# Kernel optimization log

Hardware: AMD Instinct MI355X
Metric: run time of the kernel (lower is better)

The kernel has to match this reference:

```python
import jax, jax.numpy as jnp
import numpy as np

SIGMA = 1.0  # init kwarg: Gaussian kernel width

B, P, F = 8192, 8192, 256


def setup_inputs() -> dict:
    key = jax.random.key(0)
    kx, kp = jax.random.split(key)
    x = jax.random.normal(kx, (B, F), dtype=jnp.float32)
    prototypes = jax.random.normal(kp, (P, F), dtype=jnp.float32)
    return {"x": x, "prototypes": prototypes}


def reference(x, prototypes):
    x_sq = jnp.sum(x * x, axis=-1, keepdims=True)            # [B,1]
    p_sq = jnp.sum(prototypes * prototypes, axis=-1)          # [P]
    cross = jnp.einsum('bf,pf->bp', x, prototypes)            # [B,P]
    d2 = jnp.maximum(x_sq + p_sq[None, :] - 2.0 * cross, 0.0)
    # NOTE: original takes .pow(0.5) -> euclidean NORM (despite variable name)
    dist = jnp.sqrt(d2)                                       # [B,P]
    denom = jnp.float32(2.0 * SIGMA ** 2)
    return jnp.exp(-dist / denom)
```

## Files before the change

### kernel.cpp

```cpp
#include <hip/hip_runtime.h>
#include <cstdint>
#include <cstddef>

#define B_ROWS 8192
#define P_ROWS 8192
#define FDIM   256

#define BM 128
#define BN 128
#define BK 64
#define NSTEP (FDIM / BK)

typedef __bf16  bf16x8  __attribute__((ext_vector_type(8)));
typedef float   floatx4 __attribute__((ext_vector_type(4)));

__device__ __forceinline__ unsigned short f2bf(float f) {
  unsigned int u = __float_as_uint(f);
  u += 0x7fffu + ((u >> 16) & 1u);
  return (unsigned short)(u >> 16);
}

__device__ __forceinline__ void async16(const void* g, void* l) {
  __builtin_amdgcn_global_load_lds(
      (const __attribute__((address_space(1))) void*)g,
      (__attribute__((address_space(3))) void*)l,
      16, 0, 0);
}

__global__ void __launch_bounds__(64) prep_kernel(
    const float* __restrict__ x, const float* __restrict__ p,
    unsigned short* __restrict__ xbf, unsigned short* __restrict__ pbf,
    float* __restrict__ x2, float* __restrict__ p2) {
  const int row  = blockIdx.x;
  const int lane = threadIdx.x;

  const float* src;
  unsigned short* dst;
  float* nrm;
  int r;
  if (row < B_ROWS) { src = x; dst = xbf; nrm = x2; r = row; }
  else              { src = p; dst = pbf; nrm = p2; r = row - B_ROWS; }

  const float4 v = *reinterpret_cast<const float4*>(src + (size_t)r * FDIM + lane * 4);
  float s = v.x * v.x + v.y * v.y + v.z * v.z + v.w * v.w;
  #pragma unroll
  for (int o = 32; o > 0; o >>= 1) s += __shfl_down(s, o);
  if (lane == 0) nrm[r] = s;

  ushort4 pk;
  pk.x = f2bf(v.x); pk.y = f2bf(v.y); pk.z = f2bf(v.z); pk.w = f2bf(v.w);
  *reinterpret_cast<ushort4*>(dst + (size_t)r * FDIM + lane * 4) = pk;
}

__global__ void __launch_bounds__(256) gauss_kernel(
    const unsigned short* __restrict__ xbf, const unsigned short* __restrict__ pbf,
    const float* __restrict__ x2, const float* __restrict__ p2,
    float* __restrict__ out) {
  __shared__ __align__(16) unsigned short lds_a[BM * BK];
  __shared__ __align__(16) unsigned short lds_b[BN * BK];

  const int t    = threadIdx.x;
  const int lane = t & 63;
  const int w    = t >> 6;
  const int wr   = w >> 1;
  const int wc   = w & 1;
  const int lm   = lane & 15;
  const int q    = lane >> 4;
  const int sx   = lane & 7;

  const int M0 = blockIdx.y * BM;
  const int N0 = blockIdx.x * BN;

  const unsigned short* aSrc[4];
  const unsigned short* bSrc[4];
  int ldsOff[4];
  #pragma unroll
  for (int I = 0; I < 4; ++I) {
    const int L = I * 256 + w * 64 + lane;
    const int r = L >> 3;
    const int c = L & 7;
    const int g = c ^ (r & 7);
    aSrc[I] = xbf + (size_t)(M0 + r) * FDIM + g * 8;
    bSrc[I] = pbf + (size_t)(N0 + r) * FDIM + g * 8;
    ldsOff[I] = (I * 256 + w * 64) * 8;
  }

  floatx4 acc[4][4] = {};

  for (int s = 0; s < NSTEP; ++s) {
    __syncthreads();
    #pragma unroll
    for (int I = 0; I < 4; ++I) async16(aSrc[I] + s * BK, &lds_a[ldsOff[I]]);
    #pragma unroll
    for (int I = 0; I < 4; ++I) async16(bSrc[I] + s * BK, &lds_b[ldsOff[I]]);
    __syncthreads();

    #pragma unroll
    for (int kk = 0; kk < 2; ++kk) {
      const int slot = ((kk * 4 + q) ^ sx) * 8;
      const int aoff = (wr * 64 + lm) * BK + slot;
      const int boff = (wc * 64 + lm) * BK + slot;
      bf16x8 af[4], bfr[4];
      #pragma unroll
      for (int i = 0; i < 4; ++i) af[i]  = *(const bf16x8*)&lds_a[aoff + i * 16 * BK];
      #pragma unroll
      for (int j = 0; j < 4; ++j) bfr[j] = *(const bf16x8*)&lds_b[boff + j * 16 * BK];
      #pragma unroll
      for (int i = 0; i < 4; ++i)
        #pragma unroll
        for (int j = 0; j < 4; ++j)
          acc[i][j] = __builtin_amdgcn_mfma_f32_16x16x32_bf16(af[i], bfr[j], acc[i][j], 0, 0, 0);
    }
  }

  float p2r[4];
  #pragma unroll
  for (int j = 0; j < 4; ++j) p2r[j] = p2[N0 + wc * 64 + j * 16 + lm];
  float x2r[16];
  #pragma unroll
  for (int i = 0; i < 4; ++i)
    #pragma unroll
    for (int v = 0; v < 4; ++v)
      x2r[i * 4 + v] = x2[M0 + wr * 64 + i * 16 + q * 4 + v];

  #pragma unroll
  for (int i = 0; i < 4; ++i) {
    const int mbase = M0 + wr * 64 + i * 16 + q * 4;
    #pragma unroll
    for (int v = 0; v < 4; ++v) {
      float* orow = out + (size_t)(mbase + v) * P_ROWS + N0 + wc * 64 + lm;
      #pragma unroll
      for (int j = 0; j < 4; ++j) {
        float d2 = x2r[i * 4 + v] + p2r[j] - 2.0f * acc[i][j][v];
        d2 = fmaxf(d2, 0.0f);
        const float dist = sqrtf(d2);
        orow[j * 16] = __expf(-0.5f * dist);
      }
    }
  }
}

extern "C" void kernel_launch(void* const* d_in, const int* in_sizes, int n_in,
                              void* d_out, int out_size, void* d_ws, size_t ws_size,
                              hipStream_t stream) {
  const float* x = (const float*)d_in[0];
  const float* p = (const float*)d_in[1];
  float* out = (float*)d_out;

  char* ws = (char*)d_ws;
  unsigned short* xbf = (unsigned short*)ws;
  unsigned short* pbf = (unsigned short*)(ws + (size_t)B_ROWS * FDIM * 2);
  float* x2 = (float*)(ws + (size_t)(B_ROWS + P_ROWS) * FDIM * 2);
  float* p2 = x2 + B_ROWS;

  prep_kernel<<<dim3(B_ROWS + P_ROWS), dim3(64), 0, stream>>>(x, p, xbf, pbf, x2, p2);

  dim3 grid(P_ROWS / BN, B_ROWS / BM);
  gauss_kernel<<<grid, dim3(256), 0, stream>>>(xbf, pbf, x2, p2, out);
}
```

Baseline: 302.2 us.

## Permute prototype rows for vectorized nontemporal stores and XCD-aware block swizzle

Loads B-tile rows in a permuted order so that each lane's MFMA output columns are contiguous, which lets the epilogue write float4 values with nontemporal stores instead of scalar strided stores. The x2/p2 norm loads become vector loads as well. Block indices are remapped so that blocks landing on the same XCD share M tiles for better L2 reuse. The launch bounds ask for 4 blocks per SIMD-occupancy target, which may constrain registers.

Result: no change. 300.7 us (-0.5%).

```diff
diff --git a/kernel.cpp b/kernel.cpp
--- a/kernel.cpp
+++ b/kernel.cpp
@@ -52,7 +52,7 @@
   *reinterpret_cast<ushort4*>(dst + (size_t)r * FDIM + lane * 4) = pk;
 }
 
-__global__ void __launch_bounds__(256) gauss_kernel(
+__global__ void __launch_bounds__(256, 4) gauss_kernel(
     const unsigned short* __restrict__ xbf, const unsigned short* __restrict__ pbf,
     const float* __restrict__ x2, const float* __restrict__ p2,
     float* __restrict__ out) {
@@ -68,11 +68,13 @@
   const int q    = lane >> 4;
   const int sx   = lane & 7;
 
-  const int M0 = blockIdx.y * BM;
-  const int N0 = blockIdx.x * BN;
+  const int f   = blockIdx.y * 64 + blockIdx.x;
+  const int xcd = f & 7;
+  const int i2  = f >> 3;
+  const int M0  = (xcd * 8 + (i2 & 7)) * BM;
+  const int N0  = (i2 >> 3) * BN;
 
-  const unsigned short* aSrc[4];
-  const unsigned short* bSrc[4];
+  unsigned int aOff[4], bOff[4];
   int ldsOff[4];
   #pragma unroll
   for (int I = 0; I < 4; ++I) {
@@ -80,8 +82,9 @@
     const int r = L >> 3;
     const int c = L & 7;
     const int g = c ^ (r & 7);
-    aSrc[I] = xbf + (size_t)(M0 + r) * FDIM + g * 8;
-    bSrc[I] = pbf + (size_t)(N0 + r) * FDIM + g * 8;
+    aOff[I] = (unsigned int)((M0 + r) * FDIM + g * 8);
+    const int pr = (r & 64) + 4 * (r & 15) + ((r >> 4) & 3);
+    bOff[I] = (unsigned int)((N0 + pr) * FDIM + g * 8);
     ldsOff[I] = (I * 256 + w * 64) * 8;
   }
 
@@ -90,9 +93,9 @@
   for (int s = 0; s < NSTEP; ++s) {
     __syncthreads();
     #pragma unroll
-    for (int I = 0; I < 4; ++I) async16(aSrc[I] + s * BK, &lds_a[ldsOff[I]]);
+    for (int I = 0; I < 4; ++I) async16(xbf + aOff[I] + s * BK, &lds_a[ldsOff[I]]);
     #pragma unroll
-    for (int I = 0; I < 4; ++I) async16(bSrc[I] + s * BK, &lds_b[ldsOff[I]]);
+    for (int I = 0; I < 4; ++I) async16(pbf + bOff[I] + s * BK, &lds_b[ldsOff[I]]);
     __syncthreads();
 
     #pragma unroll
@@ -113,29 +116,25 @@
     }
   }
 
-  float p2r[4];
-  #pragma unroll
-  for (int j = 0; j < 4; ++j) p2r[j] = p2[N0 + wc * 64 + j * 16 + lm];
-  float x2r[16];
-  #pragma unroll
-  for (int i = 0; i < 4; ++i)
-    #pragma unroll
-    for (int v = 0; v < 4; ++v)
-      x2r[i * 4 + v] = x2[M0 + wr * 64 + i * 16 + q * 4 + v];
+  const floatx4 p2r = *reinterpret_cast<const floatx4*>(&p2[N0 + wc * 64 + 4 * lm]);
+  const int ncol = N0 + wc * 64 + 4 * lm;
 
   #pragma unroll
   for (int i = 0; i < 4; ++i) {
     const int mbase = M0 + wr * 64 + i * 16 + q * 4;
+    const floatx4 x2v = *reinterpret_cast<const floatx4*>(&x2[mbase]);
     #pragma unroll
     for (int v = 0; v < 4; ++v) {
-      float* orow = out + (size_t)(mbase + v) * P_ROWS + N0 + wc * 64 + lm;
+      floatx4 res;
       #pragma unroll
       for (int j = 0; j < 4; ++j) {
-        float d2 = x2r[i * 4 + v] + p2r[j] - 2.0f * acc[i][j][v];
+        float d2 = x2v[v] + p2r[j] - 2.0f * acc[i][j][v];
         d2 = fmaxf(d2, 0.0f);
         const float dist = sqrtf(d2);
-        orow[j * 16] = __expf(-0.5f * dist);
+        res[j] = __expf(-0.5f * dist);
       }
+      floatx4* orow = (floatx4*)(out + (size_t)(mbase + v) * P_ROWS + ncol);
+      __builtin_nontemporal_store(res, orow);
     }
   }
 }
```

## Keep x band in registers and stream double-buffered prototype tiles across a strip

Applied to the files above, without the earlier changes.

Each block now owns a 128-row band of x, held in registers across the full K=256, and walks a 1024-column strip of prototypes. It streams 64-row prototype tiles through double-buffered LDS with async loads overlapping the MFMA work and the epilogue. Prototype rows are permuted so each lane writes a contiguous float4, using nontemporal vector stores. The aim is to cut repeated A loads and K-loop barriers and to improve output store coalescing, at the cost of higher register pressure and a smaller grid of 512 blocks.

After: 341.7 us. 1.13x slower.

```diff
diff --git a/kernel.cpp b/kernel.cpp
--- a/kernel.cpp
+++ b/kernel.cpp
@@ -6,10 +6,12 @@
 #define P_ROWS 8192
 #define FDIM   256
 
-#define BM 128
-#define BN 128
-#define BK 64
-#define NSTEP (FDIM / BK)
+#define BAND    128
+#define STRIP   1024
+#define TILE    64
+#define NTILES  (STRIP / TILE)
+#define NBANDS  (B_ROWS / BAND)
+#define NSTRIPS (P_ROWS / STRIP)
 
 typedef __bf16  bf16x8  __attribute__((ext_vector_type(8)));
 typedef float   floatx4 __attribute__((ext_vector_type(4)));
@@ -52,90 +54,112 @@
   *reinterpret_cast<ushort4*>(dst + (size_t)r * FDIM + lane * 4) = pk;
 }
 
-__global__ void __launch_bounds__(256) gauss_kernel(
+__global__ void __launch_bounds__(256, 2) gauss_kernel(
     const unsigned short* __restrict__ xbf, const unsigned short* __restrict__ pbf,
     const float* __restrict__ x2, const float* __restrict__ p2,
     float* __restrict__ out) {
-  __shared__ __align__(16) unsigned short lds_a[BM * BK];
-  __shared__ __align__(16) unsigned short lds_b[BN * BK];
+  __shared__ __align__(16) unsigned short lds_b[2][TILE * FDIM];
 
   const int t    = threadIdx.x;
   const int lane = t & 63;
   const int w    = t >> 6;
-  const int wr   = w >> 1;
-  const int wc   = w & 1;
   const int lm   = lane & 15;
   const int q    = lane >> 4;
-  const int sx   = lane & 7;
+  const int s3   = lm & 7;
 
-  const int M0 = blockIdx.y * BM;
-  const int N0 = blockIdx.x * BN;
+  const int band  = blockIdx.x & (NBANDS - 1);
+  const int strip = blockIdx.x >> 6;
+  const int M0  = band * BAND;
+  const int N0s = strip * STRIP;
 
-  const unsigned short* aSrc[4];
-  const unsigned short* bSrc[4];
-  int ldsOff[4];
+  const int rowA = M0 + w * 32 + lm;
+  bf16x8 af[2][8];
   #pragma unroll
-  for (int I = 0; I < 4; ++I) {
+  for (int i = 0; i < 2; ++i)
+    #pragma unroll
+    for (int kw = 0; kw < 8; ++kw)
+      af[i][kw] = *(const bf16x8*)&xbf[(size_t)(rowA + i * 16) * FDIM + kw * 32 + q * 8];
+
+  floatx4 x2v[2];
+  #pragma unroll
+  for (int i = 0; i < 2; ++i)
+    x2v[i] = *(const floatx4*)&x2[M0 + w * 32 + i * 16 + q * 4];
+
+  unsigned int bOff[8];
+  unsigned int ldsOff[8];
+  #pragma unroll
+  for (int I = 0; I < 8; ++I) {
     const int L = I * 256 + w * 64 + lane;
-    const int r = L >> 3;
-    const int c = L & 7;
-    const int g = c ^ (r & 7);
-    aSrc[I] = xbf + (size_t)(M0 + r) * FDIM + g * 8;
-    bSrc[I] = pbf + (size_t)(N0 + r) * FDIM + g * 8;
-    ldsOff[I] = (I * 256 + w * 64) * 8;
+    const int r = L >> 5;
+    const int c = L & 31;
+    const int g = (c & 24) | ((c ^ r) & 7);
+    const int pl = 4 * (r & 15) + (r >> 4);
+    bOff[I]   = (unsigned int)((((N0s + pl) * FDIM) + g * 8) * 2);
+    ldsOff[I] = (unsigned int)((I * 256 + w * 64) * 16);
   }
+  const char* pbfB = (const char*)pbf;
 
-  floatx4 acc[4][4] = {};
+  unsigned int oOff[2][4];
+  #pragma unroll
+  for (int i = 0; i < 2; ++i)
+    #pragma unroll
+    for (int v = 0; v < 4; ++v)
+      oOff[i][v] = (unsigned int)(((M0 + w * 32 + i * 16 + q * 4 + v) * (size_t)P_ROWS
+                                   + (N0s + 4 * lm)) * 4);
 
-  for (int s = 0; s < NSTEP; ++s) {
-    __syncthreads();
+  #pragma unroll
+  for (int I = 0; I < 8; ++I)
+    async16(pbfB + bOff[I], (char*)&lds_b[0][0] + ldsOff[I]);
+  asm volatile("s_waitcnt vmcnt(0)" ::: "memory");
+  __builtin_amdgcn_s_barrier();
+
+  for (int tt = 0; tt < NTILES; ++tt) {
+    const int cur = tt & 1;
+    const floatx4 p2r = *(const floatx4*)&p2[N0s + tt * TILE + 4 * lm];
+
+    if (tt < NTILES - 1) {
+      #pragma unroll
+      for (int I = 0; I < 8; ++I)
+        async16(pbfB + bOff[I] + (unsigned int)((tt + 1) * (TILE * FDIM * 2)),
+                (char*)&lds_b[cur ^ 1][0] + ldsOff[I]);
+    }
+
+    floatx4 acc[2][4] = {};
+    const unsigned short* lb = &lds_b[cur][0];
     #pragma unroll
-    for (int I = 0; I < 4; ++I) async16(aSrc[I] + s * BK, &lds_a[ldsOff[I]]);
-    #pragma unroll
-    for (int I = 0; I < 4; ++I) async16(bSrc[I] + s * BK, &lds_b[ldsOff[I]]);
-    __syncthreads();
+    for (int kw = 0; kw < 8; ++kw) {
+      bf16x8 bfr[4];
+      #pragma unroll
+      for (int j = 0; j < 4; ++j) {
+        const int cc = (kw * 4 + q) ^ s3;
+        bfr[j] = *(const bf16x8*)&lb[(j * 16 + lm) * FDIM + cc * 8];
+      }
+      #pragma unroll
+      for (int i = 0; i < 2; ++i)
+        #pragma unroll
+        for (int j = 0; j < 4; ++j)
+          acc[i][j] = __builtin_amdgcn_mfma_f32_16x16x32_bf16(af[i][kw], bfr[j], acc[i][j], 0, 0, 0);
+    }
 
     #pragma unroll
-    for (int kk = 0; kk < 2; ++kk) {
-      const int slot = ((kk * 4 + q) ^ sx) * 8;
-      const int aoff = (wr * 64 + lm) * BK + slot;
-      const int boff = (wc * 64 + lm) * BK + slot;
-      bf16x8 af[4], bfr[4];
+    for (int i = 0; i < 2; ++i) {
       #pragma unroll
-      for (int i = 0; i < 4; ++i) af[i]  = *(const bf16x8*)&lds_a[aoff + i * 16 * BK];
-      #pragma unroll
-      for (int j = 0; j < 4; ++j) bfr[j] = *(const bf16x8*)&lds_b[boff + j * 16 * BK];
-      #pragma unroll
-      for (int i = 0; i < 4; ++i)
+      for (int v = 0; v < 4; ++v) {
+        floatx4 res;
         #pragma unroll
-        for (int j = 0; j < 4; ++j)
-          acc[i][j] = __builtin_amdgcn_mfma_f32_16x16x32_bf16(af[i], bfr[j], acc[i][j], 0, 0, 0);
+        for (int j = 0; j < 4; ++j) {
+          float d2 = x2v[i][v] + p2r[j] - 2.0f * acc[i][j][v];
+          d2 = fmaxf(d2, 0.0f);
+          res[j] = __expf(-0.5f * sqrtf(d2));
+        }
+        __builtin_nontemporal_store(
+            res, (floatx4*)((char*)out + oOff[i][v] + (unsigned int)(tt * (TILE * 4))));
+      }
     }
-  }
 
-  float p2r[4];
-  #pragma unroll
-  for (int j = 0; j < 4; ++j) p2r[j] = p2[N0 + wc * 64 + j * 16 + lm];
-  float x2r[16];
-  #pragma unroll
-  for (int i = 0; i < 4; ++i)
-    #pragma unroll
-    for (int v = 0; v < 4; ++v)
-      x2r[i * 4 + v] = x2[M0 + wr * 64 + i * 16 + q * 4 + v];
-
-  #pragma unroll
-  for (int i = 0; i < 4; ++i) {
-    const int mbase = M0 + wr * 64 + i * 16 + q * 4;
-    #pragma unroll
-    for (int v = 0; v < 4; ++v) {
-      float* orow = out + (size_t)(mbase + v) * P_ROWS + N0 + wc * 64 + lm;
-      #pragma unroll
-      for (int j = 0; j < 4; ++j) {
-        float d2 = x2r[i * 4 + v] + p2r[j] - 2.0f * acc[i][j][v];
-        d2 = fmaxf(d2, 0.0f);
-        const float dist = sqrtf(d2);
-        orow[j * 16] = __expf(-0.5f * dist);
-      }
+    if (tt < NTILES - 1) {
+      asm volatile("s_waitcnt vmcnt(8)" ::: "memory");
+      __builtin_amdgcn_s_barrier();
     }
   }
 }
@@ -155,6 +179,5 @@
 
   prep_kernel<<<dim3(B_ROWS + P_ROWS), dim3(64), 0, stream>>>(x, p, xbf, pbf, x2, p2);
 
-  dim3 grid(P_ROWS / BN, B_ROWS / BM);
-  gauss_kernel<<<grid, dim3(256), 0, stream>>>(xbf, pbf, x2, p2, out);
+  gauss_kernel<<<dim3(NBANDS * NSTRIPS), dim3(256), 0, stream>>>(xbf, pbf, x2, p2, out);
 }
```
